# Optimization experiments

Measured on AMD Instinct MI355X. Metric: run time of the kernel, lower is better.

Reference implementation:

```python
import jax, jax.numpy as jnp
import numpy as np

BS, D_IN, D_OUT, N_MASKS = 1024, 512, 512, 8

def setup_inputs() -> dict:
    key = jax.random.key(0)
    k1, k2, k3, k4 = jax.random.split(key, 4)
    x = jax.random.normal(k1, (BS, D_IN), dtype=jnp.float32)
    state = jax.random.randint(k2, (BS,), 0, N_MASKS, dtype=jnp.int32)
    # glorot-uniform-like kernel
    limit = float(np.sqrt(6.0 / (D_IN + D_OUT)))
    kernel = jax.random.uniform(k3, (D_IN, D_OUT), dtype=jnp.float32, minval=-limit, maxval=limit)
    # binary MADE connectivity masks (0/1)
    masks = (jax.random.uniform(k4, (N_MASKS, D_IN, D_OUT)) < 0.5).astype(jnp.float32)
    return {"x": x, "state": state, "kernel": kernel, "masks": masks}

def reference(x, state, kernel, masks):
    # Math of original: out = relu(x[b] @ (kernel * masks[state[b]]))
    # Efficient form: precompute all n masked kernels (small n), batched matmul,
    # then gather per-sample result. Avoids materializing [bs, d_in, d_out].
    masked = kernel[None, :, :] * masks            # [n, d_in, d_out]
    y_all = jnp.einsum('bi,nio->bno', x, masked)   # [bs, n, d_out]
    y = jnp.take_along_axis(y_all, state[:, None, None].astype(jnp.int32), axis=1)[:, 0, :]
    return jax.nn.relu(y)
```

## Files before the change

kernel.cpp:

```cpp
#include <hip/hip_runtime.h>

#define BS 1024
#define D_IN 512
#define D_OUT 512
#define N_MASKS 8

typedef short bf16x8 __attribute__((ext_vector_type(8)));
typedef float f32x4 __attribute__((ext_vector_type(4)));


__device__ __forceinline__ ushort f2bf(float f) {
    union { float f; unsigned u; } x; x.f = f;
    unsigned r = (x.u + 0x7fffu + ((x.u >> 16) & 1u)) >> 16;
    return (ushort)r;
}

__device__ __forceinline__ bf16x8 pack8(float4 a0, float4 a1) {
    union { uint u[4]; bf16x8 v; } r;
    r.u[0] = (uint)f2bf(a0.x) | ((uint)f2bf(a0.y) << 16);
    r.u[1] = (uint)f2bf(a0.z) | ((uint)f2bf(a0.w) << 16);
    r.u[2] = (uint)f2bf(a1.x) | ((uint)f2bf(a1.y) << 16);
    r.u[3] = (uint)f2bf(a1.z) | ((uint)f2bf(a1.w) << 16);
    return r.v;
}

__global__ void __launch_bounds__(BS) sort_kernel(const int* __restrict__ state,
                                                  int* __restrict__ wsi) {
    __shared__ int cnt[N_MASKS];
    __shared__ int offs[N_MASKS + 1];
    const int tid = threadIdx.x;
    if (tid < N_MASKS) cnt[tid] = 0;
    __syncthreads();
    const int s = state[tid];
    atomicAdd(&cnt[s], 1);
    __syncthreads();
    if (tid == 0) {
        int acc = 0;
        for (int i = 0; i < N_MASKS; ++i) { offs[i] = acc; acc += cnt[i]; }
        offs[N_MASKS] = acc;
    }
    __syncthreads();
    if (tid <= N_MASKS) wsi[tid] = offs[tid];
    if (tid < N_MASKS) cnt[tid] = offs[tid];
    __syncthreads();
    const int pos = atomicAdd(&cnt[s], 1);
    wsi[16 + pos] = tid;
}

__global__ void __launch_bounds__(512, 4) fused_kernel(
    const float* __restrict__ x, const float* __restrict__ kern,
    const float* __restrict__ masks, const int* __restrict__ wsi,
    float* __restrict__ out)
{
    __shared__ ushort wlds[16 * 2 * 64 * 8];
    __shared__ float red[4][2][64][4];

    const int n   = blockIdx.x;
    const int c0g = blockIdx.y * 32;
    const int rh  = blockIdx.z;
    const int tid = threadIdx.x;
    const float* __restrict__ maskn = masks + (size_t)n * (D_IN * D_OUT);

    #pragma unroll
    for (int it = 0; it < 4; ++it) {
        const int chunk = it * 512 + tid;
        const int q = chunk & 7;
        const int p = chunk >> 3;
        const size_t gidx = (size_t)(2 * p) * D_OUT + c0g + q * 4;
        const float4 k0 = *(const float4*)&kern[gidx];
        const float4 k1 = *(const float4*)&kern[gidx + D_OUT];
        const float4 m0 = *(const float4*)&maskn[gidx];
        const float4 m1 = *(const float4*)&maskn[gidx + D_OUT];
        const int kb = p >> 4, gg = (p >> 2) & 3, h = p & 3;
        const float w0[4] = {k0.x*m0.x, k0.y*m0.y, k0.z*m0.z, k0.w*m0.w};
        const float w1[4] = {k1.x*m1.x, k1.y*m1.y, k1.z*m1.z, k1.w*m1.w};
        #pragma unroll
        for (int j = 0; j < 4; ++j) {
            const int c = q * 4 + j;
            const int slot = (kb * 2 + (c >> 4)) * 64 + gg * 16 + (c & 15);
            ((uint*)wlds)[slot * 4 + h] =
                (uint)f2bf(w0[j]) | ((uint)f2bf(w1[j]) << 16);
        }
    }

    const int off0 = wsi[n], off1 = wsi[n + 1];
    const int gcnt = off1 - off0;
    const int T  = (gcnt + 15) >> 4;
    const int Tb = (T > rh) ? ((T - rh + 1) >> 1) : 0;
    const int M  = (Tb + 3) >> 2;

    const int lane = tid & 63;
    const int wid  = tid >> 6;
    const int rtl  = wid >> 1;
    const int kh   = wid & 1;
    const int g    = lane >> 4;
    const int cl   = lane & 15;

    __syncthreads();

    for (int m = 0; m < M; ++m) {
        const int rt = rh + 2 * (rtl + 4 * m);
        const bool active = (rt < T);
        f32x4 acc0 = {0.f,0.f,0.f,0.f}, acc1 = {0.f,0.f,0.f,0.f};
        int rv = -1;
        if (active) {
            const int p = off0 + rt * 16 + cl;
            rv = (p < off1) ? wsi[16 + p] : -1;
            const float* xr = x + (size_t)(rv < 0 ? 0 : rv) * D_IN + kh * 256 + g * 8;
            #pragma unroll
            for (int i = 0; i < 8; ++i) {
                const float4 a0 = *(const float4*)(xr + i * 32);
                const float4 a1 = *(const float4*)(xr + i * 32 + 4);
                const bf16x8 a = pack8(a0, a1);
                const int kbg = kh * 8 + i;
                const bf16x8 b0 = *(const bf16x8*)&wlds[((kbg * 2 + 0) * 64 + lane) * 8];
                const bf16x8 b1 = *(const bf16x8*)&wlds[((kbg * 2 + 1) * 64 + lane) * 8];
                acc0 = __builtin_amdgcn_mfma_f32_16x16x32_bf16(a, b0, acc0, 0, 0, 0);
                acc1 = __builtin_amdgcn_mfma_f32_16x16x32_bf16(a, b1, acc1, 0, 0, 0);
            }
        }
        if (kh) {
            *(f32x4*)&red[rtl][0][lane][0] = acc0;
            *(f32x4*)&red[rtl][1][lane][0] = acc1;
        }
        __syncthreads();
        if (!kh && active) {
            acc0 += *(const f32x4*)&red[rtl][0][lane][0];
            acc1 += *(const f32x4*)&red[rtl][1][lane][0];
            #pragma unroll
            for (int r = 0; r < 4; ++r) {
                const int brow = __shfl(rv, g * 4 + r);
                if (brow >= 0) {
                    float* op = out + (size_t)brow * D_OUT + c0g;
                    op[cl]      = fmaxf(acc0[r], 0.f);
                    op[16 + cl] = fmaxf(acc1[r], 0.f);
                }
            }
        }
        __syncthreads();
    }
}

extern "C" void kernel_launch(void* const* d_in, const int* in_sizes, int n_in,
                              void* d_out, int out_size, void* d_ws, size_t ws_size,
                              hipStream_t stream) {
    const float* x     = (const float*)d_in[0];
    const int*   state = (const int*)d_in[1];
    const float* kern  = (const float*)d_in[2];
    const float* masks = (const float*)d_in[3];
    float* out = (float*)d_out;
    int*   wsi = (int*)d_ws;

    sort_kernel<<<1, BS, 0, stream>>>(state, wsi);
    dim3 grid(N_MASKS, 16, 2);
    fused_kernel<<<grid, 512, 0, stream>>>(x, kern, masks, wsi, out);
}
```

Baseline: 18.34 us.

## Narrow column tiles to 16 and cover all row tiles per block with 1024 threads

Each block now handles a 16-column slice instead of 32 and drops the two-way row split, so every block processes all row tiles of its mask group using 16 waves (8 row tiles × 2 K halves). The grid becomes 8×32 blocks of 1024 threads. Each block converts half as much masked weight into LDS, and more blocks share the weight build. In exchange, x rows are re-read and re-converted by twice as many column blocks, each wave does one MFMA per K step instead of two, and large blocks may reduce occupancy.

```diff
diff --git a/kernel.cpp b/kernel.cpp
--- a/kernel.cpp
+++ b/kernel.cpp
@@ -47,25 +47,22 @@
     wsi[16 + pos] = tid;
 }
 
-__global__ void __launch_bounds__(512, 4) fused_kernel(
+__global__ void __launch_bounds__(1024, 4) fused_kernel(
     const float* __restrict__ x, const float* __restrict__ kern,
     const float* __restrict__ masks, const int* __restrict__ wsi,
     float* __restrict__ out)
 {
-    __shared__ ushort wlds[16 * 2 * 64 * 8];
-    __shared__ float red[4][2][64][4];
+    __shared__ ushort wlds[16 * 64 * 8];
+    __shared__ float red[8][64][4];
 
     const int n   = blockIdx.x;
-    const int c0g = blockIdx.y * 32;
-    const int rh  = blockIdx.z;
+    const int c0g = blockIdx.y * 16;
     const int tid = threadIdx.x;
     const float* __restrict__ maskn = masks + (size_t)n * (D_IN * D_OUT);
 
-    #pragma unroll
-    for (int it = 0; it < 4; ++it) {
-        const int chunk = it * 512 + tid;
-        const int q = chunk & 7;
-        const int p = chunk >> 3;
+    {
+        const int q = tid & 3;
+        const int p = tid >> 2;
         const size_t gidx = (size_t)(2 * p) * D_OUT + c0g + q * 4;
         const float4 k0 = *(const float4*)&kern[gidx];
         const float4 k1 = *(const float4*)&kern[gidx + D_OUT];
@@ -77,7 +74,7 @@
         #pragma unroll
         for (int j = 0; j < 4; ++j) {
             const int c = q * 4 + j;
-            const int slot = (kb * 2 + (c >> 4)) * 64 + gg * 16 + (c & 15);
+            const int slot = kb * 64 + gg * 16 + c;
             ((uint*)wlds)[slot * 4 + h] =
                 (uint)f2bf(w0[j]) | ((uint)f2bf(w1[j]) << 16);
         }
@@ -85,9 +82,8 @@
 
     const int off0 = wsi[n], off1 = wsi[n + 1];
     const int gcnt = off1 - off0;
-    const int T  = (gcnt + 15) >> 4;
-    const int Tb = (T > rh) ? ((T - rh + 1) >> 1) : 0;
-    const int M  = (Tb + 3) >> 2;
+    const int T = (gcnt + 15) >> 4;
+    const int M = (T + 7) >> 3;
 
     const int lane = tid & 63;
     const int wid  = tid >> 6;
@@ -99,9 +95,9 @@
     __syncthreads();
 
     for (int m = 0; m < M; ++m) {
-        const int rt = rh + 2 * (rtl + 4 * m);
+        const int rt = rtl + 8 * m;
         const bool active = (rt < T);
-        f32x4 acc0 = {0.f,0.f,0.f,0.f}, acc1 = {0.f,0.f,0.f,0.f};
+        f32x4 acc = {0.f, 0.f, 0.f, 0.f};
         int rv = -1;
         if (active) {
             const int p = off0 + rt * 16 + cl;
@@ -112,28 +108,21 @@
                 const float4 a0 = *(const float4*)(xr + i * 32);
                 const float4 a1 = *(const float4*)(xr + i * 32 + 4);
                 const bf16x8 a = pack8(a0, a1);
-                const int kbg = kh * 8 + i;
-                const bf16x8 b0 = *(const bf16x8*)&wlds[((kbg * 2 + 0) * 64 + lane) * 8];
-                const bf16x8 b1 = *(const bf16x8*)&wlds[((kbg * 2 + 1) * 64 + lane) * 8];
-                acc0 = __builtin_amdgcn_mfma_f32_16x16x32_bf16(a, b0, acc0, 0, 0, 0);
-                acc1 = __builtin_amdgcn_mfma_f32_16x16x32_bf16(a, b1, acc1, 0, 0, 0);
+                const bf16x8 b = *(const bf16x8*)&wlds[(((kh * 8 + i) * 64) + lane) * 8];
+                acc = __builtin_amdgcn_mfma_f32_16x16x32_bf16(a, b, acc, 0, 0, 0);
             }
         }
         if (kh) {
-            *(f32x4*)&red[rtl][0][lane][0] = acc0;
-            *(f32x4*)&red[rtl][1][lane][0] = acc1;
+            *(f32x4*)&red[rtl][lane][0] = acc;
         }
         __syncthreads();
         if (!kh && active) {
-            acc0 += *(const f32x4*)&red[rtl][0][lane][0];
-            acc1 += *(const f32x4*)&red[rtl][1][lane][0];
+            acc += *(const f32x4*)&red[rtl][lane][0];
             #pragma unroll
             for (int r = 0; r < 4; ++r) {
                 const int brow = __shfl(rv, g * 4 + r);
                 if (brow >= 0) {
-                    float* op = out + (size_t)brow * D_OUT + c0g;
-                    op[cl]      = fmaxf(acc0[r], 0.f);
-                    op[16 + cl] = fmaxf(acc1[r], 0.f);
+                    out[(size_t)brow * D_OUT + c0g + cl] = fmaxf(acc[r], 0.f);
                 }
             }
         }
@@ -152,6 +141,6 @@
     int*   wsi = (int*)d_ws;
 
     sort_kernel<<<1, BS, 0, stream>>>(state, wsi);
-    dim3 grid(N_MASKS, 16, 2);
-    fused_kernel<<<grid, 512, 0, stream>>>(x, kern, masks, wsi, out);
+    dim3 grid(N_MASKS, 32);
+    fused_kernel<<<grid, 1024, 0, stream>>>(x, kern, masks, wsi, out);
 }
```

Result: slower. 21.72 us (+18.5%).
